# Kernel optimization log

Hardware: AMD Instinct MI355X
Metric: run time of the kernel (lower is better)

The kernel has to match this reference:

```python
import jax, jax.numpy as jnp
import numpy as np

HEADS = 16
DIM_HEAD = 64
RMS_EPS = 1e-12  # torch F.normalize default eps


def setup_inputs() -> dict:
    key = jax.random.key(0)
    k1, k2, k3 = jax.random.split(key, 3)
    b, n, dim = 2, 2048, 1024
    dim_inner = HEADS * DIM_HEAD
    x = jax.random.normal(k1, (b, n, dim), dtype=jnp.float32)
    gamma = jnp.ones((dim,), dtype=jnp.float32)
    w_qkv = jax.random.normal(k2, (dim, 3 * dim_inner), dtype=jnp.float32) * (dim ** -0.5)
    w_out = jax.random.normal(k3, (dim_inner, dim), dtype=jnp.float32) * (dim_inner ** -0.5)
    return {"x": x, "gamma": gamma, "w_qkv": w_qkv, "w_out": w_out}


def reference(x, gamma, w_qkv, w_out):
    b, n, dim = x.shape
    h, d = HEADS, DIM_HEAD
    # RMSNorm: F.normalize(x, dim=-1) * sqrt(dim) * gamma
    l2 = jnp.maximum(jnp.linalg.norm(x, axis=-1, keepdims=True), RMS_EPS)
    normed = x / l2 * (dim ** 0.5) * gamma
    # qkv projection, split order: (qkv h d)
    qkv = (normed @ w_qkv).reshape(b, n, 3, h, d)
    qkv = jnp.transpose(qkv, (2, 0, 3, 1, 4))  # [3, b, h, n, d]
    q, k, v = qkv[0], qkv[1], qkv[2]
    q = q * (d ** -0.5)
    sim = jnp.einsum('bhid,bhjd->bhij', q, k)  # [b,h,n,n]
    mask_value = -jnp.finfo(sim.dtype).max
    causal_mask = jnp.triu(jnp.ones((n, n), dtype=bool), k=1)
    sim = jnp.where(causal_mask, mask_value, sim)
    attn = jax.nn.softmax(sim, axis=-1)
    out = jnp.einsum('bhij,bhjd->bhid', attn, v)  # [b,h,n,d]
    out = jnp.transpose(out, (0, 2, 1, 3)).reshape(b, n, h * d)
    return out @ w_out
```

## Files before the change

### kernel.cpp

```cpp
#include <hip/hip_runtime.h>
#include <hip/hip_bf16.h>

#define BATCH 2
#define SEQ 2048
#define DMODEL 1024
#define NHEAD 16
#define DHEAD 64
#define NQKV 3072
#define DINNER 1024

typedef __attribute__((ext_vector_type(4))) short short4v;
typedef __attribute__((ext_vector_type(8))) short short8v;
typedef __attribute__((ext_vector_type(4))) float f32x4;

__device__ __forceinline__ unsigned short f2bf(float f) {
  union { float f; unsigned int u; } c; c.f = f;
  unsigned int u = c.u;
  u += 0x7fffu + ((u >> 16) & 1u);
  return (unsigned short)(u >> 16);
}

__device__ __forceinline__ float exp2_hw(float x) {
  float r;
  asm("v_exp_f32 %0, %1" : "=v"(r) : "v"(x));
  return r;
}

#define GL16(gp, lp)                                             \
  __builtin_amdgcn_global_load_lds(                              \
      (__attribute__((address_space(1))) void*)(gp),             \
      (__attribute__((address_space(3))) void*)(lp), 16, 0, 0)

__global__ __launch_bounds__(256) void transpose_cast_kernel(const float* __restrict__ in,
                                                             unsigned short* __restrict__ out,
                                                             int K, int N) {
  __shared__ float tile[32][33];
  const int tiles_n = N >> 5;
  const int tn = blockIdx.x % tiles_n;
  const int tk = blockIdx.x / tiles_n;
  const int k0 = tk << 5, n0 = tn << 5;
  const int t = threadIdx.x;
#pragma unroll
  for (int p = 0; p < 4; p++) {
    const int e = p * 256 + t;
    const int r = e >> 5, c = e & 31;
    tile[r][c] = in[(size_t)(k0 + r) * N + n0 + c];
  }
  __syncthreads();
#pragma unroll
  for (int p = 0; p < 4; p++) {
    const int e = p * 256 + t;
    const int r = e >> 5, c = e & 31;
    out[(size_t)(n0 + r) * K + k0 + c] = f2bf(tile[c][r]);
  }
}

__global__ __launch_bounds__(256) void rmsnorm_kernel(const float* __restrict__ x,
                                                      const float* __restrict__ gamma,
                                                      unsigned short* __restrict__ out) {
  const int row = blockIdx.x;
  const int t = threadIdx.x;
  const float* xr = x + (size_t)row * DMODEL;
  float4 v = ((const float4*)xr)[t];
  float ss = v.x * v.x + v.y * v.y + v.z * v.z + v.w * v.w;
#pragma unroll
  for (int off = 1; off < 64; off <<= 1) ss += __shfl_xor(ss, off);
  __shared__ float wss[4];
  if ((t & 63) == 0) wss[t >> 6] = ss;
  __syncthreads();
  const float tot = wss[0] + wss[1] + wss[2] + wss[3];
  float l2 = sqrtf(tot);
  l2 = fmaxf(l2, 1e-12f);
  const float s = 32.0f / l2;
  const float4 gm = ((const float4*)gamma)[t];
  unsigned short o[4];
  o[0] = f2bf(v.x * s * gm.x);
  o[1] = f2bf(v.y * s * gm.y);
  o[2] = f2bf(v.z * s * gm.z);
  o[3] = f2bf(v.w * s * gm.w);
  unsigned short* op = out + (size_t)row * DMODEL + t * 4;
  *(short4v*)op = *(short4v*)o;
}

#define BM 128
#define BN 128
#define BKT 32
#define TILE_E (BM * BKT)

__device__ void gemm_core(const unsigned short* __restrict__ A,
                          const unsigned short* __restrict__ Bt, int K, int rowBase,
                          int colBase, unsigned short* sA, unsigned short* sB,
                          f32x4 acc[4][4]) {
  const int t = threadIdx.x;
  const int lane = t & 63, wave = t >> 6;
  const int l15 = lane & 15, g = lane >> 4;
  const int wr = (wave >> 1) * 64, wc = (wave & 1) * 64;
#pragma unroll
  for (int m = 0; m < 4; m++)
#pragma unroll
    for (int n = 0; n < 4; n++) acc[m][n] = (f32x4){0.f, 0.f, 0.f, 0.f};
  const int r0 = t >> 2, o0 = (t & 3) * 8;
  const unsigned short* Ag0 = A + (size_t)(rowBase + r0) * K + o0;
  const unsigned short* Ag1 = A + (size_t)(rowBase + r0 + 64) * K + o0;
  const unsigned short* Bg0 = Bt + (size_t)(colBase + r0) * K + o0;
  const unsigned short* Bg1 = Bt + (size_t)(colBase + r0 + 64) * K + o0;
  GL16(Ag0, sA + t * 8);
  GL16(Ag1, sA + (t + 256) * 8);
  GL16(Bg0, sB + t * 8);
  GL16(Bg1, sB + (t + 256) * 8);
  __syncthreads();
  int cur = 0;
  for (int k0 = 0; k0 < K; k0 += BKT, cur ^= 1) {
    if (k0 + BKT < K) {
      const int nxto = (cur ^ 1) * TILE_E;
      GL16(Ag0 + k0 + BKT, sA + nxto + t * 8);
      GL16(Ag1 + k0 + BKT, sA + nxto + (t + 256) * 8);
      GL16(Bg0 + k0 + BKT, sB + nxto + t * 8);
      GL16(Bg1 + k0 + BKT, sB + nxto + (t + 256) * 8);
    }
    const unsigned short* sAc = sA + cur * TILE_E;
    const unsigned short* sBc = sB + cur * TILE_E;
    short8v af[4], bf[4];
#pragma unroll
    for (int m = 0; m < 4; m++)
      af[m] = *(const short8v*)(sAc + (wr + m * 16 + l15) * BKT + 8 * g);
#pragma unroll
    for (int n = 0; n < 4; n++)
      bf[n] = *(const short8v*)(sBc + (wc + n * 16 + l15) * BKT + 8 * g);
#pragma unroll
    for (int m = 0; m < 4; m++)
#pragma unroll
      for (int n = 0; n < 4; n++)
        acc[m][n] = __builtin_amdgcn_mfma_f32_16x16x32_bf16(af[m], bf[n], acc[m][n], 0, 0, 0);
    __syncthreads();
  }
}

__global__ __launch_bounds__(256) void qkv_gemm_kernel(const unsigned short* __restrict__ A,
                                                       const unsigned short* __restrict__ Bt,
                                                       unsigned short* __restrict__ qb,
                                                       unsigned short* __restrict__ kb,
                                                       unsigned short* __restrict__ vtb) {
  __shared__ __align__(16) unsigned short sA[2 * TILE_E];
  __shared__ __align__(16) unsigned short sB[2 * TILE_E];
  const int nbn = NQKV / BN;
  const int bm = blockIdx.x / nbn, bn = blockIdx.x % nbn;
  f32x4 acc[4][4];
  gemm_core(A, Bt, DMODEL, bm * BM, bn * BN, sA, sB, acc);
  const int t = threadIdx.x, lane = t & 63, wave = t >> 6;
  const int l15 = lane & 15, g = lane >> 4;
  const int wr = (wave >> 1) * 64, wc = (wave & 1) * 64;
#pragma unroll
  for (int m = 0; m < 4; m++)
#pragma unroll
    for (int n = 0; n < 4; n++) {
      const int col = bn * BN + wc + n * 16 + l15;
      const int part = col >> 10;
      const int h = (col >> 6) & 15;
      const int d = col & 63;
      const int row0 = bm * BM + wr + m * 16 + 4 * g;
      const int bb = row0 >> 11, i0 = row0 & 2047;
      if (part == 2) {
        const int ip = (i0 & ~31) | (((i0 >> 2) & 3) << 3) | (((i0 >> 4) & 1) << 2);
        union { short4v v; unsigned short u[4]; } pk;
#pragma unroll
        for (int r = 0; r < 4; r++) pk.u[r] = f2bf(acc[m][n][r]);
        *(short4v*)(vtb + ((size_t)(bb * NHEAD + h) * DHEAD + d) * SEQ + ip) = pk.v;
      } else {
#pragma unroll
        for (int r = 0; r < 4; r++) {
          const size_t idx = (((size_t)(bb * NHEAD + h)) * SEQ + i0 + r) * DHEAD + d;
          const float v = acc[m][n][r];
          if (part == 0) qb[idx] = f2bf(v * 0.18033688f);
          else kb[idx] = f2bf(v);
        }
      }
    }
}

__global__ __launch_bounds__(256) void out_gemm_kernel(const unsigned short* __restrict__ A,
                                                       const unsigned short* __restrict__ Bt,
                                                       float* __restrict__ C) {
  __shared__ __align__(16) unsigned short sA[2 * TILE_E];
  __shared__ __align__(16) unsigned short sB[2 * TILE_E];
  const int nbn = DMODEL / BN;
  const int bm = blockIdx.x / nbn, bn = blockIdx.x % nbn;
  f32x4 acc[4][4];
  gemm_core(A, Bt, DINNER, bm * BM, bn * BN, sA, sB, acc);
  const int t = threadIdx.x, lane = t & 63, wave = t >> 6;
  const int l15 = lane & 15, g = lane >> 4;
  const int wr = (wave >> 1) * 64, wc = (wave & 1) * 64;
#pragma unroll
  for (int m = 0; m < 4; m++)
#pragma unroll
    for (int n = 0; n < 4; n++) {
      const int col = bn * BN + wc + n * 16 + l15;
#pragma unroll
      for (int r = 0; r < 4; r++) {
        const int row = bm * BM + wr + m * 16 + 4 * g + r;
        C[(size_t)row * DMODEL + col] = acc[m][n][r];
      }
    }
}

__global__ __launch_bounds__(256, 4) void attn_kernel(const unsigned short* __restrict__ qb,
                                                      const unsigned short* __restrict__ kb,
                                                      const unsigned short* __restrict__ vtb,
                                                      unsigned short* __restrict__ ob) {
  __shared__ __align__(16) unsigned short sK[2][64 * 64];
  __shared__ __align__(16) unsigned short sV[2][64 * 72];
  const int t = threadIdx.x, lane = t & 63, wave = t >> 6;
  const int l15 = lane & 15, g = lane >> 4;
  const int bh = blockIdx.x & 31;
  const int qord = blockIdx.x >> 5;
  const int qblk = (qord < 8) ? 31 - qord
                 : (qord < 16) ? qord - 8
                 : (qord < 24) ? 39 - qord
                 : qord - 16;
  const int qrow = qblk * 64 + wave * 16 + l15;
  const unsigned short* qptr = qb + (size_t)bh * SEQ * DHEAD;
  const unsigned short* kptr = kb + (size_t)bh * SEQ * DHEAD;
  const unsigned short* vtptr = vtb + (size_t)bh * DHEAD * SEQ;

  const int kr0 = t >> 3, kj0 = ((t & 7) ^ (kr0 & 7)) * 8;
  const int kr1 = (t + 256) >> 3, kj1 = ((t & 7) ^ (kr1 & 7)) * 8;
  const int vr0 = t >> 3, vo0 = (t & 7) * 8;
  const int vr1 = (t + 256) >> 3, vo1 = (t & 7) * 8;

  short8v qf[2];
#pragma unroll
  for (int kk = 0; kk < 2; kk++)
    qf[kk] = *(const short8v*)(qptr + (size_t)qrow * DHEAD + kk * 32 + 8 * g);

  union { short8v v; unsigned short u[8]; } ones;
#pragma unroll
  for (int j = 0; j < 8; j++) ones.u[j] = 0x3F80;

  float rm = -__builtin_inff();
  f32x4 acc_l = (f32x4){0.f, 0.f, 0.f, 0.f};
  f32x4 acc_o[4];
#pragma unroll
  for (int df = 0; df < 4; df++) acc_o[df] = (f32x4){0.f, 0.f, 0.f, 0.f};

  const int nsteps = qblk + 1;

  GL16(kptr + (size_t)kr0 * DHEAD + kj0, sK[0] + t * 8);
  GL16(kptr + (size_t)kr1 * DHEAD + kj1, sK[0] + (t + 256) * 8);
  {
    short8v va = *(const short8v*)(vtptr + (size_t)vr0 * SEQ + vo0);
    short8v vb = *(const short8v*)(vtptr + (size_t)vr1 * SEQ + vo1);
    *(short8v*)(sV[0] + vr0 * 72 + vo0) = va;
    *(short8v*)(sV[0] + vr1 * 72 + vo1) = vb;
  }
  __syncthreads();

  int cur = 0;
  for (int s = 0; s < nsteps; ++s, cur ^= 1) {
    const int nxt = cur ^ 1;
    const bool more = (s + 1 < nsteps);
    short8v va, vb;
    if (more) {
      const int k0n = (s + 1) * 64;
      GL16(kptr + (size_t)(k0n + kr0) * DHEAD + kj0, sK[nxt] + t * 8);
      GL16(kptr + (size_t)(k0n + kr1) * DHEAD + kj1, sK[nxt] + (t + 256) * 8);
      va = *(const short8v*)(vtptr + (size_t)vr0 * SEQ + k0n + vo0);
      vb = *(const short8v*)(vtptr + (size_t)vr1 * SEQ + k0n + vo1);
    }
    {
      const int k0 = s * 64;
      const unsigned short* sKc = sK[cur];
      const unsigned short* sVc = sV[cur];
      short8v kf[4][2];
#pragma unroll
      for (int n4 = 0; n4 < 4; n4++) {
        const int row = n4 * 16 + l15;
#pragma unroll
        for (int kk = 0; kk < 2; kk++)
          kf[n4][kk] = *(const short8v*)(sKc + row * 64 + (((kk * 4 + g) ^ (row & 7)) * 8));
      }
      f32x4 s4[4];
#pragma unroll
      for (int n4 = 0; n4 < 4; n4++) s4[n4] = (f32x4){0.f, 0.f, 0.f, 0.f};
#pragma unroll
      for (int n4 = 0; n4 < 4; n4++)
#pragma unroll
        for (int kk = 0; kk < 2; kk++)
          s4[n4] = __builtin_amdgcn_mfma_f32_16x16x32_bf16(kf[n4][kk], qf[kk],
                                                           s4[n4], 0, 0, 0);
      if (s == nsteps - 1) {
#pragma unroll
        for (int n4 = 0; n4 < 4; n4++)
#pragma unroll
          for (int r = 0; r < 4; r++)
            if (k0 + n4 * 16 + 4 * g + r > qrow) s4[n4][r] = -__builtin_inff();
      }
      float mx = s4[0][0];
#pragma unroll
      for (int n4 = 0; n4 < 4; n4++)
#pragma unroll
        for (int r = 0; r < 4; r++)
          if (n4 || r) mx = fmaxf(mx, s4[n4][r]);
      if (!__all(mx <= rm)) {
        mx = fmaxf(mx, __shfl_xor(mx, 16));
        mx = fmaxf(mx, __shfl_xor(mx, 32));
        const float nm = fmaxf(rm, mx);
        const float al = exp2_hw(rm - nm);
        rm = nm;
#pragma unroll
        for (int r = 0; r < 4; r++) acc_l[r] *= al;
#pragma unroll
        for (int df = 0; df < 4; df++)
#pragma unroll
          for (int r = 0; r < 4; r++) acc_o[df][r] *= al;
      }
#pragma unroll
      for (int n4 = 0; n4 < 4; n4++)
#pragma unroll
        for (int r = 0; r < 4; r++) s4[n4][r] = exp2_hw(s4[n4][r] - rm);
      unsigned int pw[8];
#pragma unroll
      for (int n4 = 0; n4 < 4; n4++) {
        asm("v_cvt_pk_bf16_f32 %0, %1, %2"
            : "=v"(pw[n4 * 2]) : "v"(s4[n4][0]), "v"(s4[n4][1]));
        asm("v_cvt_pk_bf16_f32 %0, %1, %2"
            : "=v"(pw[n4 * 2 + 1]) : "v"(s4[n4][2]), "v"(s4[n4][3]));
      }
      union { short8v v; unsigned int wd[4]; } paA, paB;
      paA.wd[0] = pw[0]; paA.wd[1] = pw[1]; paA.wd[2] = pw[2]; paA.wd[3] = pw[3];
      paB.wd[0] = pw[4]; paB.wd[1] = pw[5]; paB.wd[2] = pw[6]; paB.wd[3] = pw[7];
      acc_l = __builtin_amdgcn_mfma_f32_16x16x32_bf16(ones.v, paA.v, acc_l, 0, 0, 0);
      acc_l = __builtin_amdgcn_mfma_f32_16x16x32_bf16(ones.v, paB.v, acc_l, 0, 0, 0);
#pragma unroll
      for (int df = 0; df < 4; df++) {
        const unsigned short* pv = sVc + (df * 16 + l15) * 72 + 8 * g;
        const short8v vfa = *(const short8v*)(pv);
        acc_o[df] = __builtin_amdgcn_mfma_f32_16x16x32_bf16(vfa, paA.v, acc_o[df], 0, 0, 0);
        const short8v vfb = *(const short8v*)(pv + 32);
        acc_o[df] = __builtin_amdgcn_mfma_f32_16x16x32_bf16(vfb, paB.v, acc_o[df], 0, 0, 0);
      }
    }
    if (more) {
      *(short8v*)(sV[nxt] + vr0 * 72 + vo0) = va;
      *(short8v*)(sV[nxt] + vr1 * 72 + vo1) = vb;
    }
    __syncthreads();
  }

  const int bb = bh >> 4, hh = bh & 15;
  const float inv = 1.0f / acc_l[0];
#pragma unroll
  for (int df = 0; df < 4; df++) {
    union { short4v v; unsigned short u[4]; } pk4;
#pragma unroll
    for (int r = 0; r < 4; r++) pk4.u[r] = f2bf(acc_o[df][r] * inv);
    *(short4v*)(ob + ((size_t)bb * SEQ + qrow) * DINNER + hh * DHEAD + df * 16 + 4 * g) =
        pk4.v;
  }
}

extern "C" void kernel_launch(void* const* d_in, const int* in_sizes, int n_in,
                              void* d_out, int out_size, void* d_ws, size_t ws_size,
                              hipStream_t stream) {
  (void)in_sizes; (void)n_in; (void)out_size; (void)ws_size;
  const float* x = (const float*)d_in[0];
  const float* gamma = (const float*)d_in[1];
  const float* w_qkv = (const float*)d_in[2];
  const float* w_out = (const float*)d_in[3];
  float* out = (float*)d_out;
  char* ws = (char*)d_ws;
  unsigned short* wqkvT = (unsigned short*)(ws);
  unsigned short* woutT = (unsigned short*)(ws + 6291456);
  unsigned short* normed = (unsigned short*)(ws + 8388608);
  unsigned short* qbuf = (unsigned short*)(ws + 16777216);
  unsigned short* kbuf = (unsigned short*)(ws + 25165824);
  unsigned short* vtbuf = (unsigned short*)(ws + 33554432);
  unsigned short* aout = (unsigned short*)(ws + 41943040);

  hipLaunchKernelGGL(transpose_cast_kernel, dim3((DMODEL / 32) * (NQKV / 32)), dim3(256), 0,
                     stream, w_qkv, wqkvT, DMODEL, NQKV);
  hipLaunchKernelGGL(transpose_cast_kernel, dim3((DINNER / 32) * (DMODEL / 32)), dim3(256), 0,
                     stream, w_out, woutT, DINNER, DMODEL);
  hipLaunchKernelGGL(rmsnorm_kernel, dim3(BATCH * SEQ), dim3(256), 0, stream, x, gamma, normed);
  hipLaunchKernelGGL(qkv_gemm_kernel, dim3((BATCH * SEQ / BM) * (NQKV / BN)), dim3(256), 0,
                     stream, normed, wqkvT, qbuf, kbuf, vtbuf);
  hipLaunchKernelGGL(attn_kernel, dim3(BATCH * NHEAD * 32), dim3(256), 0, stream,
                     qbuf, kbuf, vtbuf, aout);
  hipLaunchKernelGGL(out_gemm_kernel, dim3((BATCH * SEQ / BM) * (DMODEL / BN)), dim3(256), 0,
                     stream, aout, woutT, out);
}
```

Measured before the change: 110.6 us.

## Rewrite QKV GEMM with 256x256 tiles, 512 threads and triple-buffered async loads

Replaces the shared gemm_core in the QKV projection with a dedicated kernel. It uses 256x256 output tiles across 8 waves, a 3-stage ring of direct global-to-LDS loads with explicit vmcnt waits, and an XOR swizzle on the K chunks to reduce LDS bank conflicts. The goal is more data reuse per tile and better hiding of load latency. The trade-offs are far fewer blocks (192) for the 256 CUs, which risks underfilling the device, plus heavier register pressure from 32 accumulators per thread.

```diff
diff --git a/kernel.cpp b/kernel.cpp
--- a/kernel.cpp
+++ b/kernel.cpp
@@ -136,41 +136,104 @@
   }
 }
 
-__global__ __launch_bounds__(256) void qkv_gemm_kernel(const unsigned short* __restrict__ A,
-                                                       const unsigned short* __restrict__ Bt,
-                                                       unsigned short* __restrict__ qb,
-                                                       unsigned short* __restrict__ kb,
-                                                       unsigned short* __restrict__ vtb) {
-  __shared__ __align__(16) unsigned short sA[2 * TILE_E];
-  __shared__ __align__(16) unsigned short sB[2 * TILE_E];
-  const int nbn = NQKV / BN;
-  const int bm = blockIdx.x / nbn, bn = blockIdx.x % nbn;
-  f32x4 acc[4][4];
-  gemm_core(A, Bt, DMODEL, bm * BM, bn * BN, sA, sB, acc);
+#define QBM 256
+#define QBN 256
+#define QBK 32
+#define QTE (QBM * QBK)
+#define QNT (DMODEL / QBK)
+
+__global__ __launch_bounds__(512, 2) void qkv_gemm_kernel(const unsigned short* __restrict__ A,
+                                                          const unsigned short* __restrict__ Bt,
+                                                          unsigned short* __restrict__ qb,
+                                                          unsigned short* __restrict__ kb,
+                                                          unsigned short* __restrict__ vtb) {
+  __shared__ __align__(16) unsigned short sA[3][QTE];
+  __shared__ __align__(16) unsigned short sB[3][QTE];
   const int t = threadIdx.x, lane = t & 63, wave = t >> 6;
   const int l15 = lane & 15, g = lane >> 4;
-  const int wr = (wave >> 1) * 64, wc = (wave & 1) * 64;
-#pragma unroll
-  for (int m = 0; m < 4; m++)
-#pragma unroll
-    for (int n = 0; n < 4; n++) {
-      const int col = bn * BN + wc + n * 16 + l15;
+  const int wm = wave >> 2, wn = wave & 3;
+  const int nbn = NQKV / QBN;
+  const int bm = blockIdx.x / nbn, bn = blockIdx.x % nbn;
+  const int rowBase = bm * QBM, colBase = bn * QBN;
+  const int r0 = t >> 2, j0 = t & 3;
+  const int r1 = r0 + 128;
+  const unsigned short* Ag0 = A + (size_t)(rowBase + r0) * DMODEL + ((j0 ^ (r0 & 3)) * 8);
+  const unsigned short* Ag1 = A + (size_t)(rowBase + r1) * DMODEL + ((j0 ^ (r1 & 3)) * 8);
+  const unsigned short* Bg0 = Bt + (size_t)(colBase + r0) * DMODEL + ((j0 ^ (r0 & 3)) * 8);
+  const unsigned short* Bg1 = Bt + (size_t)(colBase + r1) * DMODEL + ((j0 ^ (r1 & 3)) * 8);
+
+  f32x4 acc[8][4];
+#pragma unroll
+  for (int mi = 0; mi < 8; mi++)
+#pragma unroll
+    for (int ni = 0; ni < 4; ni++) acc[mi][ni] = (f32x4){0.f, 0.f, 0.f, 0.f};
+
+#pragma unroll
+  for (int tt = 0; tt < 2; ++tt) {
+    GL16(Ag0 + tt * QBK, sA[tt] + t * 8);
+    GL16(Ag1 + tt * QBK, sA[tt] + (t + 512) * 8);
+    GL16(Bg0 + tt * QBK, sB[tt] + t * 8);
+    GL16(Bg1 + tt * QBK, sB[tt] + (t + 512) * 8);
+  }
+
+  for (int kt = 0; kt < QNT; ++kt) {
+    if (kt < QNT - 1) asm volatile("s_waitcnt vmcnt(4)" ::: "memory");
+    else              asm volatile("s_waitcnt vmcnt(0)" ::: "memory");
+    if (kt + 2 < QNT) {
+      const int nb = (kt + 2) % 3;
+      const int ko = (kt + 2) * QBK;
+      GL16(Ag0 + ko, sA[nb] + t * 8);
+      GL16(Ag1 + ko, sA[nb] + (t + 512) * 8);
+      GL16(Bg0 + ko, sB[nb] + t * 8);
+      GL16(Bg1 + ko, sB[nb] + (t + 512) * 8);
+    }
+    __builtin_amdgcn_s_barrier();
+    asm volatile("" ::: "memory");
+    __builtin_amdgcn_sched_barrier(0);
+    const unsigned short* sAc = sA[kt % 3];
+    const unsigned short* sBc = sB[kt % 3];
+    short8v af[8], bf[4];
+#pragma unroll
+    for (int mi = 0; mi < 8; mi++) {
+      const int row = wm * 128 + mi * 16 + l15;
+      af[mi] = *(const short8v*)(sAc + row * QBK + ((g ^ (row & 3)) * 8));
+    }
+#pragma unroll
+    for (int ni = 0; ni < 4; ni++) {
+      const int row = wn * 64 + ni * 16 + l15;
+      bf[ni] = *(const short8v*)(sBc + row * QBK + ((g ^ (row & 3)) * 8));
+    }
+    asm volatile("s_waitcnt lgkmcnt(0)" ::: "memory");
+    __builtin_amdgcn_sched_barrier(0);
+    __builtin_amdgcn_s_barrier();
+#pragma unroll
+    for (int mi = 0; mi < 8; mi++)
+#pragma unroll
+      for (int ni = 0; ni < 4; ni++)
+        acc[mi][ni] = __builtin_amdgcn_mfma_f32_16x16x32_bf16(af[mi], bf[ni], acc[mi][ni], 0, 0, 0);
+  }
+
+#pragma unroll
+  for (int mi = 0; mi < 8; mi++)
+#pragma unroll
+    for (int ni = 0; ni < 4; ni++) {
+      const int col = colBase + wn * 64 + ni * 16 + l15;
       const int part = col >> 10;
       const int h = (col >> 6) & 15;
       const int d = col & 63;
-      const int row0 = bm * BM + wr + m * 16 + 4 * g;
+      const int row0 = rowBase + wm * 128 + mi * 16 + 4 * g;
       const int bb = row0 >> 11, i0 = row0 & 2047;
       if (part == 2) {
         const int ip = (i0 & ~31) | (((i0 >> 2) & 3) << 3) | (((i0 >> 4) & 1) << 2);
         union { short4v v; unsigned short u[4]; } pk;
 #pragma unroll
-        for (int r = 0; r < 4; r++) pk.u[r] = f2bf(acc[m][n][r]);
+        for (int r = 0; r < 4; r++) pk.u[r] = f2bf(acc[mi][ni][r]);
         *(short4v*)(vtb + ((size_t)(bb * NHEAD + h) * DHEAD + d) * SEQ + ip) = pk.v;
       } else {
 #pragma unroll
         for (int r = 0; r < 4; r++) {
           const size_t idx = (((size_t)(bb * NHEAD + h)) * SEQ + i0 + r) * DHEAD + d;
-          const float v = acc[m][n][r];
+          const float v = acc[mi][ni][r];
           if (part == 0) qb[idx] = f2bf(v * 0.18033688f);
           else kb[idx] = f2bf(v);
         }
@@ -381,7 +444,7 @@
   hipLaunchKernelGGL(transpose_cast_kernel, dim3((DINNER / 32) * (DMODEL / 32)), dim3(256), 0,
                      stream, w_out, woutT, DINNER, DMODEL);
   hipLaunchKernelGGL(rmsnorm_kernel, dim3(BATCH * SEQ), dim3(256), 0, stream, x, gamma, normed);
-  hipLaunchKernelGGL(qkv_gemm_kernel, dim3((BATCH * SEQ / BM) * (NQKV / BN)), dim3(256), 0,
+  hipLaunchKernelGGL(qkv_gemm_kernel, dim3((BATCH * SEQ / QBM) * (NQKV / QBN)), dim3(512), 0,
                      stream, normed, wqkvT, qbuf, kbuf, vtbuf);
   hipLaunchKernelGGL(attn_kernel, dim3(BATCH * NHEAD * 32), dim3(256), 0, stream,
                      qbuf, kbuf, vtbuf, aout);
```

New measurement: 119.0 us. 1.08x slower.

## Use triple-buffered LDS ring with swizzled layout in projection GEMMs

Applied to the files above, without the earlier changes.

Replaces the double-buffered GEMM main loop with a three-stage LDS ring that prefetches two K-tiles ahead. Explicit vmcnt waits let one tile's loads stay in flight across the barrier. LDS chunk addresses are XOR-swizzled to reduce bank conflicts on the fragment reads, and MFMA issue is wrapped in s_setprio. This uses more shared memory per block (launch bounds drop to 3 blocks), and correctness relies on the hand-counted vmcnt values matching the compiler's emitted loads.

```diff
diff --git a/kernel.cpp b/kernel.cpp
--- a/kernel.cpp
+++ b/kernel.cpp
@@ -86,11 +86,12 @@
 #define BN 128
 #define BKT 32
 #define TILE_E (BM * BKT)
-
-__device__ void gemm_core(const unsigned short* __restrict__ A,
-                          const unsigned short* __restrict__ Bt, int K, int rowBase,
-                          int colBase, unsigned short* sA, unsigned short* sB,
-                          f32x4 acc[4][4]) {
+#define RNT (DMODEL / BKT)
+
+__device__ void gemm_ring(const unsigned short* __restrict__ A,
+                          const unsigned short* __restrict__ Bt, int rowBase,
+                          int colBase, unsigned short (*sA)[TILE_E],
+                          unsigned short (*sB)[TILE_E], f32x4 acc[4][4]) {
   const int t = threadIdx.x;
   const int lane = t & 63, wave = t >> 6;
   const int l15 = lane & 15, g = lane >> 4;
@@ -99,54 +100,74 @@
   for (int m = 0; m < 4; m++)
 #pragma unroll
     for (int n = 0; n < 4; n++) acc[m][n] = (f32x4){0.f, 0.f, 0.f, 0.f};
-  const int r0 = t >> 2, o0 = (t & 3) * 8;
-  const unsigned short* Ag0 = A + (size_t)(rowBase + r0) * K + o0;
-  const unsigned short* Ag1 = A + (size_t)(rowBase + r0 + 64) * K + o0;
-  const unsigned short* Bg0 = Bt + (size_t)(colBase + r0) * K + o0;
-  const unsigned short* Bg1 = Bt + (size_t)(colBase + r0 + 64) * K + o0;
-  GL16(Ag0, sA + t * 8);
-  GL16(Ag1, sA + (t + 256) * 8);
-  GL16(Bg0, sB + t * 8);
-  GL16(Bg1, sB + (t + 256) * 8);
-  __syncthreads();
-  int cur = 0;
-  for (int k0 = 0; k0 < K; k0 += BKT, cur ^= 1) {
-    if (k0 + BKT < K) {
-      const int nxto = (cur ^ 1) * TILE_E;
-      GL16(Ag0 + k0 + BKT, sA + nxto + t * 8);
-      GL16(Ag1 + k0 + BKT, sA + nxto + (t + 256) * 8);
-      GL16(Bg0 + k0 + BKT, sB + nxto + t * 8);
-      GL16(Bg1 + k0 + BKT, sB + nxto + (t + 256) * 8);
-    }
-    const unsigned short* sAc = sA + cur * TILE_E;
-    const unsigned short* sBc = sB + cur * TILE_E;
+  const int r0 = t >> 2, j0 = t & 3;
+  const int swz = (r0 >> 1) & 3;
+  const unsigned short* Ag0 = A + (size_t)(rowBase + r0) * DMODEL + ((j0 ^ swz) * 8);
+  const unsigned short* Ag1 = A + (size_t)(rowBase + r0 + 64) * DMODEL + ((j0 ^ swz) * 8);
+  const unsigned short* Bg0 = Bt + (size_t)(colBase + r0) * DMODEL + ((j0 ^ swz) * 8);
+  const unsigned short* Bg1 = Bt + (size_t)(colBase + r0 + 64) * DMODEL + ((j0 ^ swz) * 8);
+
+#pragma unroll
+  for (int tt = 0; tt < 2; ++tt) {
+    GL16(Ag0 + tt * BKT, sA[tt] + t * 8);
+    GL16(Ag1 + tt * BKT, sA[tt] + (t + 256) * 8);
+    GL16(Bg0 + tt * BKT, sB[tt] + t * 8);
+    GL16(Bg1 + tt * BKT, sB[tt] + (t + 256) * 8);
+  }
+  asm volatile("s_waitcnt vmcnt(4)" ::: "memory");
+  __builtin_amdgcn_sched_barrier(0);
+  __builtin_amdgcn_s_barrier();
+
+  for (int kt = 0; kt < RNT; ++kt) {
+    const unsigned short* sAc = sA[kt % 3];
+    const unsigned short* sBc = sB[kt % 3];
+    const bool pf = (kt + 2 < RNT);
+    if (pf) {
+      const int nb = (kt + 2) % 3;
+      const int ko = (kt + 2) * BKT;
+      GL16(Ag0 + ko, sA[nb] + t * 8);
+      GL16(Ag1 + ko, sA[nb] + (t + 256) * 8);
+      GL16(Bg0 + ko, sB[nb] + t * 8);
+      GL16(Bg1 + ko, sB[nb] + (t + 256) * 8);
+    }
     short8v af[4], bf[4];
 #pragma unroll
-    for (int m = 0; m < 4; m++)
-      af[m] = *(const short8v*)(sAc + (wr + m * 16 + l15) * BKT + 8 * g);
-#pragma unroll
-    for (int n = 0; n < 4; n++)
-      bf[n] = *(const short8v*)(sBc + (wc + n * 16 + l15) * BKT + 8 * g);
+    for (int m = 0; m < 4; m++) {
+      const int row = wr + m * 16 + l15;
+      af[m] = *(const short8v*)(sAc + row * BKT + ((g ^ ((row >> 1) & 3)) * 8));
+    }
+#pragma unroll
+    for (int n = 0; n < 4; n++) {
+      const int row = wc + n * 16 + l15;
+      bf[n] = *(const short8v*)(sBc + row * BKT + ((g ^ ((row >> 1) & 3)) * 8));
+    }
+    asm volatile("s_waitcnt lgkmcnt(0)" ::: "memory");
+    __builtin_amdgcn_sched_barrier(0);
+    __builtin_amdgcn_s_setprio(1);
 #pragma unroll
     for (int m = 0; m < 4; m++)
 #pragma unroll
       for (int n = 0; n < 4; n++)
         acc[m][n] = __builtin_amdgcn_mfma_f32_16x16x32_bf16(af[m], bf[n], acc[m][n], 0, 0, 0);
-    __syncthreads();
-  }
-}
-
-__global__ __launch_bounds__(256) void qkv_gemm_kernel(const unsigned short* __restrict__ A,
-                                                       const unsigned short* __restrict__ Bt,
-                                                       unsigned short* __restrict__ qb,
-                                                       unsigned short* __restrict__ kb,
-                                                       unsigned short* __restrict__ vtb) {
-  __shared__ __align__(16) unsigned short sA[2 * TILE_E];
-  __shared__ __align__(16) unsigned short sB[2 * TILE_E];
+    __builtin_amdgcn_s_setprio(0);
+    if (pf) asm volatile("s_waitcnt vmcnt(4)" ::: "memory");
+    else    asm volatile("s_waitcnt vmcnt(0)" ::: "memory");
+    __builtin_amdgcn_sched_barrier(0);
+    __builtin_amdgcn_s_barrier();
+  }
+}
+
+__global__ __launch_bounds__(256, 3) void qkv_gemm_kernel(const unsigned short* __restrict__ A,
+                                                          const unsigned short* __restrict__ Bt,
+                                                          unsigned short* __restrict__ qb,
+                                                          unsigned short* __restrict__ kb,
+                                                          unsigned short* __restrict__ vtb) {
+  __shared__ __align__(16) unsigned short sA[3][TILE_E];
+  __shared__ __align__(16) unsigned short sB[3][TILE_E];
   const int nbn = NQKV / BN;
   const int bm = blockIdx.x / nbn, bn = blockIdx.x % nbn;
   f32x4 acc[4][4];
-  gemm_core(A, Bt, DMODEL, bm * BM, bn * BN, sA, sB, acc);
+  gemm_ring(A, Bt, bm * BM, bn * BN, sA, sB, acc);
   const int t = threadIdx.x, lane = t & 63, wave = t >> 6;
   const int l15 = lane & 15, g = lane >> 4;
   const int wr = (wave >> 1) * 64, wc = (wave & 1) * 64;
@@ -178,15 +199,15 @@
     }
 }
 
-__global__ __launch_bounds__(256) void out_gemm_kernel(const unsigned short* __restrict__ A,
-                                                       const unsigned short* __restrict__ Bt,
-                                                       float* __restrict__ C) {
-  __shared__ __align__(16) unsigned short sA[2 * TILE_E];
-  __shared__ __align__(16) unsigned short sB[2 * TILE_E];
+__global__ __launch_bounds__(256, 3) void out_gemm_kernel(const unsigned short* __restrict__ A,
+                                                          const unsigned short* __restrict__ Bt,
+                                                          float* __restrict__ C) {
+  __shared__ __align__(16) unsigned short sA[3][TILE_E];
+  __shared__ __align__(16) unsigned short sB[3][TILE_E];
   const int nbn = DMODEL / BN;
   const int bm = blockIdx.x / nbn, bn = blockIdx.x % nbn;
   f32x4 acc[4][4];
-  gemm_core(A, Bt, DINNER, bm * BM, bn * BN, sA, sB, acc);
+  gemm_ring(A, Bt, bm * BM, bn * BN, sA, sB, acc);
   const int t = threadIdx.x, lane = t & 63, wave = t >> 6;
   const int l15 = lane & 15, g = lane >> 4;
   const int wr = (wave >> 1) * 64, wc = (wave & 1) * 64;
```

After: 114.5 us. 1.04x slower.
